# Kernel optimization log

Hardware: AMD Instinct MI355X
Metric: run time of the kernel (lower is better)

Reference implementation:

```python
import jax, jax.numpy as jnp
import numpy as np

B, N, D, H = 8, 1024, 512, 8  # batch, num_nodes, dim, num_heads
HD = D // H                    # head_dim = 64
N_VALID = 896                  # last 128 nodes per graph are padding


def setup_inputs() -> dict:
    key = jax.random.key(0)
    ks = jax.random.split(key, 6)
    x = jax.random.normal(ks[0], (B, N, D), dtype=jnp.float32)
    # boolean validity mask: some padding nodes so mask-fill / nan_to_num paths are hit
    mask = np.ones((B, N), dtype=bool)
    mask[:, N_VALID:] = False
    node_valid_mask = jnp.asarray(mask)
    attn_bias = jax.random.normal(ks[1], (B, H, N, N), dtype=jnp.float32) * 0.1
    # torch nn.Linear convention: y = x @ W.T + b
    qkv_w = jax.random.normal(ks[2], (3 * D, D), dtype=jnp.float32) * (D ** -0.5)
    qkv_b = jax.random.normal(ks[3], (3 * D,), dtype=jnp.float32) * 0.02
    out_w = jax.random.normal(ks[4], (D, D), dtype=jnp.float32) * (D ** -0.5)
    out_b = jax.random.normal(ks[5], (D,), dtype=jnp.float32) * 0.02
    return {"x": x, "node_valid_mask": node_valid_mask, "attn_bias": attn_bias,
            "qkv_w": qkv_w, "qkv_b": qkv_b, "out_w": out_w, "out_b": out_b}


def reference(x, node_valid_mask, attn_bias, qkv_w, qkv_b, out_w, out_b):
    b, n, d = x.shape
    scale = HD ** -0.5
    # qkv projection -> [3, B, H, N, HD]
    qkv = (x @ qkv_w.T + qkv_b).reshape(b, n, 3, H, HD).transpose(2, 0, 3, 1, 4)
    q, k, v = qkv[0], qkv[1], qkv[2]
    scores = jnp.einsum('bhqd,bhkd->bhqk', q, k) * scale + attn_bias  # [B,H,N,N]
    # pair mask: both query and key node must be valid
    pair_mask = node_valid_mask[:, :, None] & node_valid_mask[:, None, :]  # [B,N,N]
    scores = jnp.where(pair_mask[:, None, :, :], scores, -jnp.inf)
    attn = jax.nn.softmax(scores, axis=-1)
    # fully-masked query rows produce NaN -> zero, matching torch.nan_to_num
    attn = jnp.nan_to_num(attn, nan=0.0, posinf=0.0, neginf=0.0)
    out = jnp.einsum('bhqk,bhkd->bhqd', attn, v)        # [B,H,N,HD]
    out = out.transpose(0, 2, 1, 3).reshape(b, n, d)     # [B,N,D]
    return out @ out_w.T + out_b
```

## Files before the change

### kernel.cpp

```cpp
#include <hip/hip_runtime.h>
#include <math.h>

constexpr int Bc  = 8;
constexpr int Nn  = 1024;
constexpr int Dd  = 512;
constexpr int Hh  = 8;
constexpr int HD  = 64;
constexpr float SCALE = 0.125f;

typedef unsigned short ushort_t;
typedef unsigned int uint32;
typedef __attribute__((ext_vector_type(8))) short short8;
typedef __attribute__((ext_vector_type(4))) float f32x4;

__device__ __forceinline__ uint32 bf16rn(float x) {
  uint32 u = __float_as_uint(x);
  return (u + 0x7FFFu + ((u >> 16) & 1u)) >> 16;
}
__device__ __forceinline__ float bf16up(uint32 h) { return __uint_as_float(h << 16); }

__device__ __forceinline__ void split8(const float* xs, uint4& hi, uint4& lo) {
  uint32 h[8], l[8];
#pragma unroll
  for (int j = 0; j < 8; ++j) {
    h[j] = bf16rn(xs[j]);
    l[j] = bf16rn(xs[j] - bf16up(h[j]));
  }
  hi.x = h[0] | (h[1] << 16); hi.y = h[2] | (h[3] << 16);
  hi.z = h[4] | (h[5] << 16); hi.w = h[6] | (h[7] << 16);
  lo.x = l[0] | (l[1] << 16); lo.y = l[2] | (l[3] << 16);
  lo.z = l[4] | (l[5] << 16); lo.w = l[6] | (l[7] << 16);
}

__device__ __forceinline__ bool lane_valid(const unsigned char* m8, bool bytelay, int idx) {
  if (bytelay) return m8[idx] != 0;
  return ((const int*)m8)[idx] != 0;
}

__global__ __launch_bounds__(256) void convert_split(
    const float* __restrict__ src, ushort_t* __restrict__ dst)
{
  const int t    = blockIdx.x * 256 + threadIdx.x;
  const int lane = t & 63;
  const int blk  = t >> 6;
  const int rt   = blk >> 4, ks = blk & 15;
  const int row  = rt * 16 + (lane & 15);
  const int k    = ks * 32 + (lane >> 4) * 8;

  const float* s = src + (size_t)row * 512 + k;
  float4 a = *(const float4*)s, b = *(const float4*)(s + 4);
  float xs[8] = {a.x, a.y, a.z, a.w, b.x, b.y, b.z, b.w};
  uint4 hi, lo; split8(xs, hi, lo);

  ushort_t* d = dst + (size_t)blk * 1024 + lane * 8;
  *(uint4*)d = hi;
  *(uint4*)(d + 512) = lo;
}

template<bool SCATTER>
__global__ __launch_bounds__(256) void gemm_x3(
    const ushort_t* __restrict__ Ac, const float* __restrict__ W,
    const float* __restrict__ bias, float* __restrict__ C, int Ncols,
    float* __restrict__ qb, float* __restrict__ kb, float* __restrict__ vb)
{
  __shared__ ushort_t Ablk[8 * 1024];
  __shared__ ushort_t Bblk[8 * 1024];

  const int t    = threadIdx.x;
  const int lane = t & 63, w = t >> 6;
  const int wr   = w >> 1, wc = w & 1;
  const int j0   = blockIdx.x * 128, i0 = blockIdx.y * 128;
  const int srow = t >> 2, skc = t & 3;

  f32x4 acc[4][4];
#pragma unroll
  for (int a = 0; a < 4; ++a)
#pragma unroll
    for (int b = 0; b < 4; ++b) acc[a][b] = (f32x4){0.f, 0.f, 0.f, 0.f};

  for (int kt = 0; kt < 16; ++kt) {
    __syncthreads();
#pragma unroll
    for (int i = 0; i < 4; ++i) {
      const int c = w * 4 + i, rt = c >> 1, hl = c & 1;
      const size_t goff =
          ((size_t)((i0 >> 4) + rt) * 16 + kt) * 1024 + hl * 512 + lane * 8;
      *(uint4*)&Ablk[rt * 1024 + hl * 512 + lane * 8] = *(const uint4*)&Ac[goff];
    }
#pragma unroll
    for (int p = 0; p < 2; ++p) {
      const int row = p * 64 + srow;
      const float* s = W + (size_t)(j0 + row) * 512 + kt * 32 + skc * 8;
      float4 w0 = *(const float4*)s, w1 = *(const float4*)(s + 4);
      float xs[8] = {w0.x, w0.y, w0.z, w0.w, w1.x, w1.y, w1.z, w1.w};
      uint4 hi, lo; split8(xs, hi, lo);
      ushort_t* d = &Bblk[(row >> 4) * 1024 + ((row & 15) + 16 * skc) * 8];
      *(uint4*)d = hi;
      *(uint4*)(d + 512) = lo;
    }
    __syncthreads();

    const ushort_t* Ab = &Ablk[(wr * 4) * 1024 + lane * 8];
    const ushort_t* Bb = &Bblk[(wc * 4) * 1024 + lane * 8];
    short8 Ah[4], Al[4];
#pragma unroll
    for (int ti = 0; ti < 4; ++ti) {
      Ah[ti] = *(const short8*)(Ab + ti * 1024);
      Al[ti] = *(const short8*)(Ab + ti * 1024 + 512);
    }
#pragma unroll
    for (int ct = 0; ct < 4; ++ct) {
      short8 Bh = *(const short8*)(Bb + ct * 1024);
      short8 Bl = *(const short8*)(Bb + ct * 1024 + 512);
#pragma unroll
      for (int ti = 0; ti < 4; ++ti) {
        acc[ti][ct] = __builtin_amdgcn_mfma_f32_16x16x32_bf16(Ah[ti], Bh, acc[ti][ct], 0, 0, 0);
        acc[ti][ct] = __builtin_amdgcn_mfma_f32_16x16x32_bf16(Al[ti], Bh, acc[ti][ct], 0, 0, 0);
        acc[ti][ct] = __builtin_amdgcn_mfma_f32_16x16x32_bf16(Ah[ti], Bl, acc[ti][ct], 0, 0, 0);
      }
    }
  }

  const int rbase = i0 + wr * 64 + (lane >> 4) * 4;
  const int cbase = j0 + wc * 64 + (lane & 15);
#pragma unroll
  for (int ct = 0; ct < 4; ++ct) {
    const int col = cbase + ct * 16;
    const float bv = bias[col];
    float* dst = nullptr; int dcol = col;
    if (SCATTER) {
      const int s = col >> 9, h = (col >> 6) & 7;
      dst  = (s == 0) ? qb : (s == 1) ? kb : vb;
      dcol = col & 63;
      dst += (size_t)h * Nn * HD + dcol;
    }
#pragma unroll
    for (int ti = 0; ti < 4; ++ti) {
      const int r0 = rbase + ti * 16;
#pragma unroll
      for (int r = 0; r < 4; ++r) {
        const float v = acc[ti][ct][r] + bv;
        const int row = r0 + r;
        if (SCATTER) {
          const int b2 = row >> 10, n = row & 1023;
          dst[((size_t)b2 * Hh * Nn + n) * HD] = v;
        } else {
          C[(size_t)row * Ncols + col] = v;
        }
      }
    }
  }
}

__global__ __launch_bounds__(256) void attn_k(
    const float* __restrict__ qg, const float* __restrict__ kg,
    const float* __restrict__ vg, const float* __restrict__ bias,
    const unsigned char* __restrict__ m8, float* __restrict__ outp)
{
  __shared__ float Qst[64][68];
  __shared__ float KP[64][68];
  __shared__ float Vst[64][68];

  const int t  = threadIdx.x;
  const int tx = t & 15;
  const int ty = t >> 4;
  const int bx = blockIdx.x;
  const int qt = bx & 15;
  const int bh = bx >> 4;
  const int b  = bh >> 3;
  const int h  = bh & 7;
  const int q0 = qt * 64;
  const bool bytelay = (m8[1] != 0);

#pragma unroll
  for (int i = 0; i < 4; ++i) {
    const int idx = i * 256 + t;
    const int qq  = idx >> 4;
    const int d4  = (idx & 15) * 4;
    float4 v = *(const float4*)&qg[((size_t)bh * Nn + q0 + qq) * HD + d4];
    Qst[d4 + 0][qq] = v.x; Qst[d4 + 1][qq] = v.y;
    Qst[d4 + 2][qq] = v.z; Qst[d4 + 3][qq] = v.w;
  }

  float O[4][4];
  float m_run[4], l_run[4];
#pragma unroll
  for (int ii = 0; ii < 4; ++ii) {
    m_run[ii] = -__builtin_inff(); l_run[ii] = 0.f;
#pragma unroll
    for (int jj = 0; jj < 4; ++jj) O[ii][jj] = 0.f;
  }

  for (int kt = 0; kt < 16; ++kt) {
    bool kv[4]; int any = 0;
#pragma unroll
    for (int jj = 0; jj < 4; ++jj) {
      kv[jj] = lane_valid(m8, bytelay, b * Nn + kt * 64 + 4 * tx + jj);
      any |= (int)kv[jj];
    }
    if (!__syncthreads_or(any)) continue;

#pragma unroll
    for (int i = 0; i < 4; ++i) {
      const int idx = i * 256 + t;
      const int kk  = idx >> 4;
      const int d4  = (idx & 15) * 4;
      float4 kvv = *(const float4*)&kg[((size_t)bh * Nn + kt * 64 + kk) * HD + d4];
      KP[d4 + 0][kk] = kvv.x; KP[d4 + 1][kk] = kvv.y;
      KP[d4 + 2][kk] = kvv.z; KP[d4 + 3][kk] = kvv.w;
      *(float4*)&Vst[kk][d4] =
          *(const float4*)&vg[((size_t)bh * Nn + kt * 64 + kk) * HD + d4];
    }
    __syncthreads();

    float4 bias4[4];
#pragma unroll
    for (int ii = 0; ii < 4; ++ii)
      bias4[ii] = *(const float4*)
          &bias[((size_t)bh * Nn + q0 + 4 * ty + ii) * Nn + kt * 64 + 4 * tx];

    float S[4][4];
#pragma unroll
    for (int ii = 0; ii < 4; ++ii)
#pragma unroll
      for (int jj = 0; jj < 4; ++jj) S[ii][jj] = 0.f;
#pragma unroll 4
    for (int d = 0; d < 64; ++d) {
      float4 q4 = *(const float4*)&Qst[d][4 * ty];
      float4 k4 = *(const float4*)&KP[d][4 * tx];
      float qa[4] = {q4.x, q4.y, q4.z, q4.w};
      float ka[4] = {k4.x, k4.y, k4.z, k4.w};
#pragma unroll
      for (int ii = 0; ii < 4; ++ii)
#pragma unroll
        for (int jj = 0; jj < 4; ++jj)
          S[ii][jj] += qa[ii] * ka[jj];
    }

    float mt[4];
#pragma unroll
    for (int ii = 0; ii < 4; ++ii) {
      float bb[4] = {bias4[ii].x, bias4[ii].y, bias4[ii].z, bias4[ii].w};
      float m = -__builtin_inff();
#pragma unroll
      for (int jj = 0; jj < 4; ++jj) {
        float s = kv[jj] ? S[ii][jj] * SCALE + bb[jj] : -__builtin_inff();
        S[ii][jj] = s;
        m = fmaxf(m, s);
      }
      mt[ii] = m;
    }
#pragma unroll
    for (int off = 1; off < 16; off <<= 1)
#pragma unroll
      for (int ii = 0; ii < 4; ++ii)
        mt[ii] = fmaxf(mt[ii], __shfl_xor(mt[ii], off));

    float alpha[4], lt[4];
#pragma unroll
    for (int ii = 0; ii < 4; ++ii) {
      float mn = fmaxf(m_run[ii], mt[ii]);
      alpha[ii] = __expf(m_run[ii] - mn);
      m_run[ii] = mn;
      float l = 0.f;
#pragma unroll
      for (int jj = 0; jj < 4; ++jj) {
        float p = __expf(S[ii][jj] - mn);
        S[ii][jj] = p;
        l += p;
      }
      lt[ii] = l;
    }
#pragma unroll
    for (int off = 1; off < 16; off <<= 1)
#pragma unroll
      for (int ii = 0; ii < 4; ++ii)
        lt[ii] += __shfl_xor(lt[ii], off);
#pragma unroll
    for (int ii = 0; ii < 4; ++ii) {
      l_run[ii] = l_run[ii] * alpha[ii] + lt[ii];
#pragma unroll
      for (int jj = 0; jj < 4; ++jj) O[ii][jj] *= alpha[ii];
    }

    __syncthreads();
#pragma unroll
    for (int jj = 0; jj < 4; ++jj) {
      float4 p4; p4.x = S[0][jj]; p4.y = S[1][jj]; p4.z = S[2][jj]; p4.w = S[3][jj];
      *(float4*)&KP[4 * tx + jj][4 * ty] = p4;
    }
    __syncthreads();

#pragma unroll 4
    for (int k = 0; k < 64; ++k) {
      float4 p4 = *(const float4*)&KP[k][4 * ty];
      float4 v4 = *(const float4*)&Vst[k][4 * tx];
      float pa[4] = {p4.x, p4.y, p4.z, p4.w};
      float va[4] = {v4.x, v4.y, v4.z, v4.w};
#pragma unroll
      for (int ii = 0; ii < 4; ++ii)
#pragma unroll
        for (int jj = 0; jj < 4; ++jj)
          O[ii][jj] += pa[ii] * va[jj];
    }
  }

#pragma unroll
  for (int ii = 0; ii < 4; ++ii) {
    const int q = q0 + 4 * ty + ii;
    const bool vq = lane_valid(m8, bytelay, b * Nn + q);
    const float r = (vq && l_run[ii] > 0.f) ? (1.f / l_run[ii]) : 0.f;
    float4 o;
    o.x = O[ii][0] * r; o.y = O[ii][1] * r;
    o.z = O[ii][2] * r; o.w = O[ii][3] * r;
    *(float4*)&outp[((size_t)(b * Nn + q)) * Dd + h * HD + 4 * tx] = o;
  }
}

extern "C" void kernel_launch(void* const* d_in, const int* in_sizes, int n_in,
                              void* d_out, int out_size, void* d_ws, size_t ws_size,
                              hipStream_t stream) {
  const float* x        = (const float*)d_in[0];
  const unsigned char* mask8 = (const unsigned char*)d_in[1];
  const float* attnbias = (const float*)d_in[2];
  const float* qkv_w    = (const float*)d_in[3];
  const float* qkv_b    = (const float*)d_in[4];
  const float* out_w    = (const float*)d_in[5];
  const float* out_b    = (const float*)d_in[6];
  float* out = (float*)d_out;

  float* ws = (float*)d_ws;
  const size_t SEG = (size_t)Bc * Hh * Nn * HD;
  ushort_t* x_conv    = (ushort_t*)ws;
  float*    qbuf      = ws + SEG;
  float*    kbuf      = ws + 2 * SEG;
  float*    vbuf      = ws + 3 * SEG;
  float*    aout      = ws;
  ushort_t* aout_conv = (ushort_t*)(ws + SEG);

  convert_split<<<8192 * 64 / 256, 256, 0, stream>>>(x, x_conv);

  gemm_x3<true><<<dim3(1536 / 128, 8192 / 128), 256, 0, stream>>>(
      x_conv, qkv_w, qkv_b, nullptr, 1536, qbuf, kbuf, vbuf);

  attn_k<<<dim3(Bc * Hh * (Nn / 64)), 256, 0, stream>>>(
      qbuf, kbuf, vbuf, attnbias, mask8, aout);

  convert_split<<<8192 * 64 / 256, 256, 0, stream>>>(aout, aout_conv);

  gemm_x3<false><<<dim3(512 / 128, 8192 / 128), 256, 0, stream>>>(
      aout_conv, out_w, out_b, out, 512, nullptr, nullptr, nullptr);
}
```

Measured before the change: 652.2 us.

## Move attention matmuls to split-bf16 MFMA with pre-fragmented Q/K/V

Replaces the scalar FP32 attention kernel with one that runs QK^T and PV on bf16 MFMA instructions. Each value is split into hi and lo bf16 parts and combined with three MFMAs to stay close to fp32 accuracy. Three new conversion kernels pre-pack Q, K and V into MFMA fragment layout in the workspace. Each wave then handles 16 query rows independently, reading fragments straight from global memory and passing P through a per-wave LDS buffer with no block-wide syncs. The cost is extra conversion kernel launches, extra global traffic for the hi/lo copies, and reliance on L2 to serve K/V fragments shared across waves.

```diff
diff --git a/kernel.cpp b/kernel.cpp
--- a/kernel.cpp
+++ b/kernel.cpp
@@ -55,6 +55,50 @@
   ushort_t* d = dst + (size_t)blk * 1024 + lane * 8;
   *(uint4*)d = hi;
   *(uint4*)(d + 512) = lo;
+}
+
+__global__ __launch_bounds__(256) void convert_frag_qk(
+    const float* __restrict__ src, ushort_t* __restrict__ dst)
+{
+  const int t    = blockIdx.x * 256 + threadIdx.x;
+  const int lane = t & 63;
+  const int fid  = t >> 6;
+  const int tile = fid >> 1, ks = fid & 1;
+  const int row  = tile * 16 + (lane & 15);
+  const int d    = ks * 32 + (lane >> 4) * 8;
+
+  const float* s = src + (size_t)row * HD + d;
+  float4 a = *(const float4*)s, b = *(const float4*)(s + 4);
+  float xs[8] = {a.x, a.y, a.z, a.w, b.x, b.y, b.z, b.w};
+  uint4 hi, lo; split8(xs, hi, lo);
+
+  ushort_t* dp = dst + (size_t)fid * 1024 + lane * 8;
+  *(uint4*)dp = hi;
+  *(uint4*)(dp + 512) = lo;
+}
+
+__global__ __launch_bounds__(256) void convert_frag_v(
+    const float* __restrict__ src, ushort_t* __restrict__ dst)
+{
+  const int t    = blockIdx.x * 256 + threadIdx.x;
+  const int lane = t & 63;
+  const int fid  = t >> 6;
+  const int dt   = fid & 3;
+  const int ks   = (fid >> 2) & 1;
+  const int kt   = (fid >> 3) & 15;
+  const int bh   = fid >> 7;
+  const int d    = dt * 16 + (lane & 15);
+  const int key0 = kt * 64 + ks * 32 + (lane >> 4) * 8;
+
+  const float* s = src + ((size_t)bh * Nn + key0) * HD + d;
+  float xs[8];
+#pragma unroll
+  for (int j = 0; j < 8; ++j) xs[j] = s[(size_t)j * HD];
+  uint4 hi, lo; split8(xs, hi, lo);
+
+  ushort_t* dp = dst + (size_t)fid * 1024 + lane * 8;
+  *(uint4*)dp = hi;
+  *(uint4*)(dp + 512) = lo;
 }
 
 template<bool SCATTER>
@@ -127,12 +171,11 @@
   for (int ct = 0; ct < 4; ++ct) {
     const int col = cbase + ct * 16;
     const float bv = bias[col];
-    float* dst = nullptr; int dcol = col;
+    float* dst = nullptr;
     if (SCATTER) {
       const int s = col >> 9, h = (col >> 6) & 7;
       dst  = (s == 0) ? qb : (s == 1) ? kb : vb;
-      dcol = col & 63;
-      dst += (size_t)h * Nn * HD + dcol;
+      dst += (size_t)h * Nn * HD + (col & 63);
     }
 #pragma unroll
     for (int ti = 0; ti < 4; ++ti) {
@@ -152,168 +195,152 @@
   }
 }
 
-__global__ __launch_bounds__(256) void attn_k(
-    const float* __restrict__ qg, const float* __restrict__ kg,
-    const float* __restrict__ vg, const float* __restrict__ bias,
+__global__ __launch_bounds__(256) void attn_mfma(
+    const ushort_t* __restrict__ qf, const ushort_t* __restrict__ kf,
+    const ushort_t* __restrict__ vf, const float* __restrict__ bias,
     const unsigned char* __restrict__ m8, float* __restrict__ outp)
 {
-  __shared__ float Qst[64][68];
-  __shared__ float KP[64][68];
-  __shared__ float Vst[64][68];
-
-  const int t  = threadIdx.x;
-  const int tx = t & 15;
-  const int ty = t >> 4;
-  const int bx = blockIdx.x;
-  const int qt = bx & 15;
-  const int bh = bx >> 4;
-  const int b  = bh >> 3;
-  const int h  = bh & 7;
-  const int q0 = qt * 64;
+  __shared__ ushort_t Pbuf[4][2048];
+
+  const int t    = threadIdx.x;
+  const int lane = t & 63, w = t >> 6;
+  const int bx   = blockIdx.x;
+  const int qt   = bx & 15;
+  const int bh   = bx >> 4;
+  const int b    = bh >> 3, h = bh & 7;
+  const int tt   = qt * 4 + w;
+  const int q0   = tt * 16;
   const bool bytelay = (m8[1] != 0);
 
-#pragma unroll
-  for (int i = 0; i < 4; ++i) {
-    const int idx = i * 256 + t;
-    const int qq  = idx >> 4;
-    const int d4  = (idx & 15) * 4;
-    float4 v = *(const float4*)&qg[((size_t)bh * Nn + q0 + qq) * HD + d4];
-    Qst[d4 + 0][qq] = v.x; Qst[d4 + 1][qq] = v.y;
-    Qst[d4 + 2][qq] = v.z; Qst[d4 + 3][qq] = v.w;
-  }
-
-  float O[4][4];
+  short8 Qh[2], Ql[2];
+#pragma unroll
+  for (int ks = 0; ks < 2; ++ks) {
+    const ushort_t* qp = qf + ((size_t)(bh * 64 + tt) * 2 + ks) * 1024 + lane * 8;
+    Qh[ks] = *(const short8*)qp;
+    Ql[ks] = *(const short8*)(qp + 512);
+  }
+
+  f32x4 Oacc[4];
+#pragma unroll
+  for (int dt = 0; dt < 4; ++dt) Oacc[dt] = (f32x4){0.f, 0.f, 0.f, 0.f};
   float m_run[4], l_run[4];
 #pragma unroll
-  for (int ii = 0; ii < 4; ++ii) {
-    m_run[ii] = -__builtin_inff(); l_run[ii] = 0.f;
-#pragma unroll
-    for (int jj = 0; jj < 4; ++jj) O[ii][jj] = 0.f;
-  }
+  for (int r = 0; r < 4; ++r) { m_run[r] = -__builtin_inff(); l_run[r] = 0.f; }
+
+  ushort_t* pb = &Pbuf[w][0];
 
   for (int kt = 0; kt < 16; ++kt) {
-    bool kv[4]; int any = 0;
-#pragma unroll
-    for (int jj = 0; jj < 4; ++jj) {
-      kv[jj] = lane_valid(m8, bytelay, b * Nn + kt * 64 + 4 * tx + jj);
-      any |= (int)kv[jj];
-    }
-    if (!__syncthreads_or(any)) continue;
-
-#pragma unroll
-    for (int i = 0; i < 4; ++i) {
-      const int idx = i * 256 + t;
-      const int kk  = idx >> 4;
-      const int d4  = (idx & 15) * 4;
-      float4 kvv = *(const float4*)&kg[((size_t)bh * Nn + kt * 64 + kk) * HD + d4];
-      KP[d4 + 0][kk] = kvv.x; KP[d4 + 1][kk] = kvv.y;
-      KP[d4 + 2][kk] = kvv.z; KP[d4 + 3][kk] = kvv.w;
-      *(float4*)&Vst[kk][d4] =
-          *(const float4*)&vg[((size_t)bh * Nn + kt * 64 + kk) * HD + d4];
-    }
-    __syncthreads();
-
-    float4 bias4[4];
-#pragma unroll
-    for (int ii = 0; ii < 4; ++ii)
-      bias4[ii] = *(const float4*)
-          &bias[((size_t)bh * Nn + q0 + 4 * ty + ii) * Nn + kt * 64 + 4 * tx];
-
-    float S[4][4];
-#pragma unroll
-    for (int ii = 0; ii < 4; ++ii)
-#pragma unroll
-      for (int jj = 0; jj < 4; ++jj) S[ii][jj] = 0.f;
-#pragma unroll 4
-    for (int d = 0; d < 64; ++d) {
-      float4 q4 = *(const float4*)&Qst[d][4 * ty];
-      float4 k4 = *(const float4*)&KP[d][4 * tx];
-      float qa[4] = {q4.x, q4.y, q4.z, q4.w};
-      float ka[4] = {k4.x, k4.y, k4.z, k4.w};
-#pragma unroll
-      for (int ii = 0; ii < 4; ++ii)
-#pragma unroll
-        for (int jj = 0; jj < 4; ++jj)
-          S[ii][jj] += qa[ii] * ka[jj];
-    }
-
-    float mt[4];
-#pragma unroll
-    for (int ii = 0; ii < 4; ++ii) {
-      float bb[4] = {bias4[ii].x, bias4[ii].y, bias4[ii].z, bias4[ii].w};
-      float m = -__builtin_inff();
-#pragma unroll
-      for (int jj = 0; jj < 4; ++jj) {
-        float s = kv[jj] ? S[ii][jj] * SCALE + bb[jj] : -__builtin_inff();
-        S[ii][jj] = s;
-        m = fmaxf(m, s);
-      }
-      mt[ii] = m;
+    const bool kvme = lane_valid(m8, bytelay, b * Nn + kt * 64 + lane);
+    const unsigned long long kmask = __ballot(kvme);
+    if (kmask == 0ull) continue;
+
+    const float* bp = bias + ((size_t)bh * Nn + q0 + (lane >> 4) * 4) * Nn
+                           + kt * 64 + (lane & 15);
+    float bias_v[4][4];
+#pragma unroll
+    for (int r = 0; r < 4; ++r)
+#pragma unroll
+      for (int nt = 0; nt < 4; ++nt)
+        bias_v[nt][r] = bp[(size_t)r * Nn + nt * 16];
+
+    f32x4 Sacc[4];
+#pragma unroll
+    for (int nt = 0; nt < 4; ++nt) Sacc[nt] = (f32x4){0.f, 0.f, 0.f, 0.f};
+#pragma unroll
+    for (int ks = 0; ks < 2; ++ks)
+#pragma unroll
+      for (int nt = 0; nt < 4; ++nt) {
+        const ushort_t* kp =
+            kf + ((size_t)(bh * 64 + kt * 4 + nt) * 2 + ks) * 1024 + lane * 8;
+        short8 Kh = *(const short8*)kp;
+        short8 Kl = *(const short8*)(kp + 512);
+        Sacc[nt] = __builtin_amdgcn_mfma_f32_16x16x32_bf16(Qh[ks], Kh, Sacc[nt], 0, 0, 0);
+        Sacc[nt] = __builtin_amdgcn_mfma_f32_16x16x32_bf16(Ql[ks], Kh, Sacc[nt], 0, 0, 0);
+        Sacc[nt] = __builtin_amdgcn_mfma_f32_16x16x32_bf16(Qh[ks], Kl, Sacc[nt], 0, 0, 0);
+      }
+
+    float Sv[4][4];
+    float mt[4] = {-__builtin_inff(), -__builtin_inff(), -__builtin_inff(), -__builtin_inff()};
+#pragma unroll
+    for (int nt = 0; nt < 4; ++nt) {
+      const bool kv = (kmask >> (nt * 16 + (lane & 15))) & 1ull;
+#pragma unroll
+      for (int r = 0; r < 4; ++r) {
+        float s = kv ? Sacc[nt][r] * SCALE + bias_v[nt][r] : -__builtin_inff();
+        Sv[nt][r] = s;
+        mt[r] = fmaxf(mt[r], s);
+      }
     }
 #pragma unroll
     for (int off = 1; off < 16; off <<= 1)
 #pragma unroll
-      for (int ii = 0; ii < 4; ++ii)
-        mt[ii] = fmaxf(mt[ii], __shfl_xor(mt[ii], off));
+      for (int r = 0; r < 4; ++r) mt[r] = fmaxf(mt[r], __shfl_xor(mt[r], off));
 
     float alpha[4], lt[4];
 #pragma unroll
-    for (int ii = 0; ii < 4; ++ii) {
-      float mn = fmaxf(m_run[ii], mt[ii]);
-      alpha[ii] = __expf(m_run[ii] - mn);
-      m_run[ii] = mn;
-      float l = 0.f;
-#pragma unroll
-      for (int jj = 0; jj < 4; ++jj) {
-        float p = __expf(S[ii][jj] - mn);
-        S[ii][jj] = p;
-        l += p;
-      }
-      lt[ii] = l;
+    for (int r = 0; r < 4; ++r) {
+      const float mn = fmaxf(m_run[r], mt[r]);
+      alpha[r] = __expf(m_run[r] - mn);
+      m_run[r] = mn;
+      lt[r] = 0.f;
+    }
+#pragma unroll
+    for (int nt = 0; nt < 4; ++nt) {
+      const int ksp    = nt >> 1;
+      const int key_in = (nt & 1) * 16 + (lane & 15);
+      const int lane_p = 16 * (key_in >> 3);
+      const int j      = key_in & 7;
+#pragma unroll
+      for (int r = 0; r < 4; ++r) {
+        const float p = __expf(Sv[nt][r] - m_run[r]);
+        lt[r] += p;
+        const uint32 ph = bf16rn(p);
+        const uint32 pl = bf16rn(p - bf16up(ph));
+        const int lp = ((lane >> 4) * 4 + r) + lane_p;
+        pb[(ksp * 2 + 0) * 512 + lp * 8 + j] = (ushort_t)ph;
+        pb[(ksp * 2 + 1) * 512 + lp * 8 + j] = (ushort_t)pl;
+      }
     }
 #pragma unroll
     for (int off = 1; off < 16; off <<= 1)
 #pragma unroll
-      for (int ii = 0; ii < 4; ++ii)
-        lt[ii] += __shfl_xor(lt[ii], off);
-#pragma unroll
-    for (int ii = 0; ii < 4; ++ii) {
-      l_run[ii] = l_run[ii] * alpha[ii] + lt[ii];
-#pragma unroll
-      for (int jj = 0; jj < 4; ++jj) O[ii][jj] *= alpha[ii];
-    }
-
-    __syncthreads();
-#pragma unroll
-    for (int jj = 0; jj < 4; ++jj) {
-      float4 p4; p4.x = S[0][jj]; p4.y = S[1][jj]; p4.z = S[2][jj]; p4.w = S[3][jj];
-      *(float4*)&KP[4 * tx + jj][4 * ty] = p4;
-    }
-    __syncthreads();
-
-#pragma unroll 4
-    for (int k = 0; k < 64; ++k) {
-      float4 p4 = *(const float4*)&KP[k][4 * ty];
-      float4 v4 = *(const float4*)&Vst[k][4 * tx];
-      float pa[4] = {p4.x, p4.y, p4.z, p4.w};
-      float va[4] = {v4.x, v4.y, v4.z, v4.w};
-#pragma unroll
-      for (int ii = 0; ii < 4; ++ii)
-#pragma unroll
-        for (int jj = 0; jj < 4; ++jj)
-          O[ii][jj] += pa[ii] * va[jj];
-    }
-  }
-
-#pragma unroll
-  for (int ii = 0; ii < 4; ++ii) {
-    const int q = q0 + 4 * ty + ii;
+      for (int r = 0; r < 4; ++r) lt[r] += __shfl_xor(lt[r], off);
+#pragma unroll
+    for (int r = 0; r < 4; ++r) l_run[r] = l_run[r] * alpha[r] + lt[r];
+#pragma unroll
+    for (int dt = 0; dt < 4; ++dt)
+#pragma unroll
+      for (int r = 0; r < 4; ++r) Oacc[dt][r] *= alpha[r];
+
+    short8 Ph[2], Pl[2];
+#pragma unroll
+    for (int ks = 0; ks < 2; ++ks) {
+      Ph[ks] = *(const short8*)&pb[(ks * 2 + 0) * 512 + lane * 8];
+      Pl[ks] = *(const short8*)&pb[(ks * 2 + 1) * 512 + lane * 8];
+    }
+
+#pragma unroll
+    for (int dt = 0; dt < 4; ++dt)
+#pragma unroll
+      for (int ks = 0; ks < 2; ++ks) {
+        const ushort_t* vp =
+            vf + ((size_t)(((bh * 16 + kt) * 2 + ks) * 4 + dt)) * 1024 + lane * 8;
+        short8 Vh = *(const short8*)vp;
+        short8 Vl = *(const short8*)(vp + 512);
+        Oacc[dt] = __builtin_amdgcn_mfma_f32_16x16x32_bf16(Ph[ks], Vh, Oacc[dt], 0, 0, 0);
+        Oacc[dt] = __builtin_amdgcn_mfma_f32_16x16x32_bf16(Pl[ks], Vh, Oacc[dt], 0, 0, 0);
+        Oacc[dt] = __builtin_amdgcn_mfma_f32_16x16x32_bf16(Ph[ks], Vl, Oacc[dt], 0, 0, 0);
+      }
+  }
+
+#pragma unroll
+  for (int r = 0; r < 4; ++r) {
+    const int q = q0 + (lane >> 4) * 4 + r;
     const bool vq = lane_valid(m8, bytelay, b * Nn + q);
-    const float r = (vq && l_run[ii] > 0.f) ? (1.f / l_run[ii]) : 0.f;
-    float4 o;
-    o.x = O[ii][0] * r; o.y = O[ii][1] * r;
-    o.z = O[ii][2] * r; o.w = O[ii][3] * r;
-    *(float4*)&outp[((size_t)(b * Nn + q)) * Dd + h * HD + 4 * tx] = o;
+    const float rinv = (vq && l_run[r] > 0.f) ? (1.f / l_run[r]) : 0.f;
+    float* op = outp + ((size_t)(b * Nn + q)) * Dd + h * HD + (lane & 15);
+#pragma unroll
+    for (int dt = 0; dt < 4; ++dt) op[dt * 16] = Oacc[dt][r] * rinv;
   }
 }
 
@@ -331,23 +358,34 @@
 
   float* ws = (float*)d_ws;
   const size_t SEG = (size_t)Bc * Hh * Nn * HD;
-  ushort_t* x_conv    = (ushort_t*)ws;
-  float*    qbuf      = ws + SEG;
-  float*    kbuf      = ws + 2 * SEG;
-  float*    vbuf      = ws + 3 * SEG;
-  float*    aout      = ws;
-  ushort_t* aout_conv = (ushort_t*)(ws + SEG);
-
-  convert_split<<<8192 * 64 / 256, 256, 0, stream>>>(x, x_conv);
-
-  gemm_x3<true><<<dim3(1536 / 128, 8192 / 128), 256, 0, stream>>>(
+  float* A = ws;
+  float* B = ws + SEG;
+  float* C = ws + 2 * SEG;
+  float* D = ws + 3 * SEG;
+
+  ushort_t* x_conv    = (ushort_t*)A;
+  float*    qbuf      = B;
+  float*    kbuf      = C;
+  float*    vbuf      = D;
+  ushort_t* qfrag     = (ushort_t*)A;
+  ushort_t* kfrag     = (ushort_t*)B;
+  ushort_t* vfrag     = (ushort_t*)C;
+  float*    aout      = D;
+  ushort_t* aout_conv = (ushort_t*)A;
+
+  convert_split<<<2048, 256, 0, stream>>>(x, x_conv);
+
+  gemm_x3<true><<<dim3(12, 64), 256, 0, stream>>>(
       x_conv, qkv_w, qkv_b, nullptr, 1536, qbuf, kbuf, vbuf);
 
-  attn_k<<<dim3(Bc * Hh * (Nn / 64)), 256, 0, stream>>>(
-      qbuf, kbuf, vbuf, attnbias, mask8, aout);
-
-  convert_split<<<8192 * 64 / 256, 256, 0, stream>>>(aout, aout_conv);
-
-  gemm_x3<false><<<dim3(512 / 128, 8192 / 128), 256, 0, stream>>>(
+  convert_frag_qk<<<2048, 256, 0, stream>>>(qbuf, qfrag);
+  convert_frag_qk<<<2048, 256, 0, stream>>>(kbuf, kfrag);
+  convert_frag_v <<<2048, 256, 0, stream>>>(vbuf, vfrag);
+
+  attn_mfma<<<1024, 256, 0, stream>>>(
+      qfrag, kfrag, vfrag, attnbias, mask8, aout);
+
+  convert_split<<<2048, 256, 0, stream>>>(aout, aout_conv);
+  gemm_x3<false><<<dim3(4, 64), 256, 0, stream>>>(
       aout_conv, out_w, out_b, out, 512, nullptr, nullptr, nullptr);
 }
```

Result: faster. 566.9 us (-13.1%).
